# Performance work log

Measured on AMD Instinct MI355X. Metric: run time of the kernel, lower is better.

## Reference

```python
import jax, jax.numpy as jnp
import numpy as np

B, T, NIN, N, NOUT = 64, 512, 64, 1024, 32
DT, TAU = 1.0, 10.0
STATE_STD, RATE_STD, OUT_STD = 0.05, 0.05, 0.05
HIDDEN_G = 1.0


def retanh(x):
    return jnp.maximum(jnp.tanh(x), 0.0)


def setup_inputs() -> dict:
    key = jax.random.key(0)
    ks = jax.random.split(key, 10)
    u = jax.random.normal(ks[0], (B, T, NIN), jnp.float32)
    x_0 = jnp.zeros((N,), jnp.float32)
    state_noise = STATE_STD * jax.random.normal(ks[1], (B, T, N), jnp.float32)
    rate_noise = RATE_STD * jax.random.normal(ks[2], (B, T, N), jnp.float32)
    output_noise = OUT_STD * jax.random.normal(ks[3], (B, T, NOUT), jnp.float32)
    W_in = jax.random.normal(ks[4], (N, NIN), jnp.float32) / np.sqrt(NIN).astype(np.float32)
    b_in = 0.1 + 0.01 * jax.random.normal(ks[5], (N,), jnp.float32)
    W_rec = jax.random.normal(ks[6], (N, N), jnp.float32) * (HIDDEN_G / np.sqrt(N).astype(np.float32))
    W_rec = W_rec * (1.0 - jnp.eye(N, dtype=jnp.float32))  # zero self-connections
    lim = 1.0 / np.sqrt(N).astype(np.float32)
    W_out = jax.random.uniform(ks[7], (NOUT, N), jnp.float32, -lim, lim)
    b_out = jax.random.uniform(ks[8], (NOUT,), jnp.float32, -lim, lim)
    return {"u": u, "x_0": x_0, "state_noise": state_noise, "rate_noise": rate_noise,
            "output_noise": output_noise, "W_in": W_in, "b_in": b_in, "W_rec": W_rec,
            "W_out": W_out, "b_out": b_out}


def reference(u, x_0, state_noise, rate_noise, output_noise, W_in, b_in, W_rec, W_out, b_out):
    alpha = DT / TAU
    # time-major for scan: [T, B, ...]
    u_t = jnp.swapaxes(u, 0, 1)
    sn = jnp.swapaxes(state_noise, 0, 1)
    rn = jnp.swapaxes(rate_noise, 0, 1)
    on = jnp.swapaxes(output_noise, 0, 1)
    x0 = jnp.broadcast_to(x_0, (B, N))
    r0 = retanh(x0)

    def step(carry, inp):
        x, r = carry
        ut, snt, rnt, ont = inp
        x_next = x + alpha * (-x + r @ W_rec.T + ut @ W_in.T + b_in + snt)
        r_next = retanh(x_next) + rnt
        z_next = r_next @ W_out.T + b_out + ont
        return (x_next, r_next), (x_next, r_next, z_next)

    _, (X, R, Z) = jax.lax.scan(step, (x0, r0), (u_t, sn, rn, on))
    # back to batch-major [B, T, ...]
    return (jnp.swapaxes(X, 0, 1), jnp.swapaxes(R, 0, 1), jnp.swapaxes(Z, 0, 1))
```

## Files before the change

kernel.cpp:

```cpp
#include <hip/hip_runtime.h>
#include <hip/hip_bf16.h>
#include <stdint.h>

#define B_    64
#define T_    512
#define NIN_  64
#define N_    1024
#define NOUT_ 32

#define NISL  16
#define BPI   16
#define MB    4
#define COLS  64
#define NT    4
#define KW    256
#define KT    8

#define MAIL_WORDS (NISL * BPI * BPI)

typedef float f32x4 __attribute__((ext_vector_type(4)));
typedef short s16x8 __attribute__((ext_vector_type(8)));

__device__ __forceinline__ unsigned short f2bf(float f) {
  union { float f; unsigned u; } v; v.f = f;
  unsigned r = v.u + 0x7FFFu + ((v.u >> 16) & 1u);
  return (unsigned short)(r >> 16);
}

__device__ __forceinline__ s16x8 cvt8(float4 a, float4 b) {
  s16x8 f;
  f[0] = (short)f2bf(a.x); f[1] = (short)f2bf(a.y);
  f[2] = (short)f2bf(a.z); f[3] = (short)f2bf(a.w);
  f[4] = (short)f2bf(b.x); f[5] = (short)f2bf(b.y);
  f[6] = (short)f2bf(b.z); f[7] = (short)f2bf(b.w);
  return f;
}

#define LD16S(dst, base, OFF) \
  asm volatile("global_load_dwordx4 %0, %1, off offset:" #OFF " sc0 sc1" \
               : "=v"(dst) : "v"(base) : "memory")
#define LDALLS() do { \
  LD16S(afr[0], bp, 0);   LD16S(afr[1], bp, 64);  \
  LD16S(afr[2], bp, 128); LD16S(afr[3], bp, 192); \
  LD16S(afr[4], bp, 256); LD16S(afr[5], bp, 320); \
  LD16S(afr[6], bp, 384); LD16S(afr[7], bp, 448); } while (0)

__global__ __launch_bounds__(256, 1) void rnn_scan(
    const float* __restrict__ U, const float* __restrict__ X0,
    const float* __restrict__ SN, const float* __restrict__ RN,
    const float* __restrict__ Wi, const float* __restrict__ Bi,
    const float* __restrict__ Wr,
    float* __restrict__ X, float* __restrict__ R,
    unsigned* __restrict__ mail, unsigned* __restrict__ ex)
{
  const int bid   = blockIdx.x;
  const int isl   = bid / BPI, slice = bid % BPI;
  const int tid   = threadIdx.x;
  const int wave  = tid >> 6, lane = tid & 63;
  const int l15   = lane & 15, koct = lane >> 4;
  const int colbase = slice * COLS;

  s16x8 bfrag[KT][NT];
#pragma unroll
  for (int kt = 0; kt < KT; ++kt) {
    const int k0 = wave * KW + kt * 32 + koct * 8;
#pragma unroll
    for (int nt = 0; nt < NT; ++nt) {
      const float4* q = (const float4*)(Wr + (size_t)(colbase + nt * 16 + l15) * N_ + k0);
      bfrag[kt][nt] = cvt8(q[0], q[1]);
    }
  }
  s16x8 wifrag[NT];
  if (wave < 2) {
#pragma unroll
    for (int nt = 0; nt < NT; ++nt) {
      const float4* q = (const float4*)(Wi + (size_t)(colbase + nt * 16 + l15) * NIN_ + wave * 32 + koct * 8);
      wifrag[nt] = cvt8(q[0], q[1]);
    }
  }

  const int cc   = lane;
  const int bloc = wave;
  const int bg   = isl * MB + bloc;
  const int nn   = colbase + cc;
  const int abatch = isl * MB + (l15 & 3);

  float x = X0[nn];
  const float bin = Bi[nn];
  const float r0 = fmaxf(tanhf(x), 0.f);

  __shared__ float part[4][COLS][MB];

  const unsigned* const myline = mail + (isl * BPI + slice) * BPI;
  unsigned* const postcol      = mail + isl * BPI * BPI + slice;

  {
    unsigned short h = f2bf(r0);
    unsigned other = __shfl_xor((unsigned)h, 1);
    unsigned vv  = (unsigned)h | (other << 16);
    unsigned vv2 = __shfl_xor(vv, 2);
    if ((lane & 3) == 0) {
      uint64_t q8 = (uint64_t)vv | ((uint64_t)vv2 << 32);
      __hip_atomic_store((uint64_t*)(ex + (size_t)bg * (N_ / 2) + (nn >> 1)), q8,
                         __ATOMIC_RELAXED, __HIP_MEMORY_SCOPE_AGENT);
    }
  }
  __syncthreads();
  if (tid < BPI)
    __hip_atomic_store(postcol + tid * BPI, 1u,
                       __ATOMIC_RELAXED, __HIP_MEMORY_SCOPE_AGENT);

  float pxn = 0.f, prv = 0.f;

  for (int t = 0; t < T_; ++t) {
    const int par = t & 1;
    const size_t row = (size_t)bg * T_ + t;

    const float snv = SN[row * N_ + nn];
    const float rnv = RN[row * N_ + nn];
    float4 uq0, uq1;
    if (wave < 2) {
      const float4* q = (const float4*)(U + ((size_t)(isl * MB + (l15 & 3)) * T_ + t) * NIN_
                                          + wave * 32 + koct * 8);
      uq0 = q[0]; uq1 = q[1];
    }

    {
      const unsigned need = (unsigned)(t + 1);
      for (;;) {
        unsigned fv = __hip_atomic_load(myline + l15, __ATOMIC_RELAXED,
                                        __HIP_MEMORY_SCOPE_AGENT);
        if (__all((int)(fv >= need))) break;
        __builtin_amdgcn_s_sleep(1);
      }
    }

    if (t > 0) {
      X[(row - 1) * N_ + nn] = pxn;
      R[(row - 1) * N_ + nn] = prv;
    }

    const unsigned* bp = ex + (size_t)par * (B_ * (N_ / 2))
                            + (size_t)abatch * (N_ / 2)
                            + ((wave * KW + koct * 8) >> 1);
    s16x8 afr[KT];
    LDALLS();
    asm volatile("s_waitcnt vmcnt(0)" ::: "memory");
    __builtin_amdgcn_sched_barrier(0);

    f32x4 acc[NT];
#pragma unroll
    for (int nt = 0; nt < NT; ++nt) acc[nt] = f32x4{0.f, 0.f, 0.f, 0.f};
#pragma unroll
    for (int kt = 0; kt < KT; ++kt)
#pragma unroll
      for (int nt = 0; nt < NT; ++nt)
        acc[nt] = __builtin_amdgcn_mfma_f32_16x16x32_bf16(afr[kt], bfrag[kt][nt], acc[nt], 0, 0, 0);
    if (wave < 2) {
      s16x8 ua = cvt8(uq0, uq1);
#pragma unroll
      for (int nt = 0; nt < NT; ++nt)
        acc[nt] = __builtin_amdgcn_mfma_f32_16x16x32_bf16(ua, wifrag[nt], acc[nt], 0, 0, 0);
    }

    if (lane < 16) {
#pragma unroll
      for (int nt = 0; nt < NT; ++nt) {
        const int s = (nt * 2 + (lane >> 3)) & 3;
        f32x4 a = acc[nt];
        if (s & 1) a = f32x4{a[1], a[0], a[3], a[2]};
        if (s & 2) a = f32x4{a[2], a[3], a[0], a[1]};
        *(f32x4*)&part[wave][nt * 16 + lane][0] = a;
      }
    }
    __syncthreads();
    const int sr = (cc >> 3) & 3;
    const float mat = part[0][cc][bloc ^ sr] + part[1][cc][bloc ^ sr] +
                      part[2][cc][bloc ^ sr] + part[3][cc][bloc ^ sr];
    const float xn = x + 0.1f * (-x + mat + bin + snv);
    const float rv = fmaxf(tanhf(xn), 0.f) + rnv;
    x = xn;

    {
      unsigned short h = f2bf(rv);
      unsigned other = __shfl_xor((unsigned)h, 1);
      unsigned vv  = (unsigned)h | (other << 16);
      unsigned vv2 = __shfl_xor(vv, 2);
      if ((lane & 3) == 0) {
        uint64_t q8 = (uint64_t)vv | ((uint64_t)vv2 << 32);
        __hip_atomic_store((uint64_t*)(ex + (size_t)(par ^ 1) * (B_ * (N_ / 2)) +
                                       (size_t)bg * (N_ / 2) + (nn >> 1)), q8,
                           __ATOMIC_RELAXED, __HIP_MEMORY_SCOPE_AGENT);
      }
    }
    __syncthreads();
    if (tid < BPI)
      __hip_atomic_store(postcol + tid * BPI, (unsigned)(t + 2),
                         __ATOMIC_RELAXED, __HIP_MEMORY_SCOPE_AGENT);

    pxn = xn; prv = rv;
  }
  {
    const size_t lrow = (size_t)bg * T_ + (T_ - 1);
    X[lrow * N_ + nn] = pxn;
    R[lrow * N_ + nn] = prv;
  }
}

#define TCH 64
__global__ __launch_bounds__(256, 2) void rnn_zout(
    const float* __restrict__ Rm, const float* __restrict__ ON,
    const float* __restrict__ Wo, const float* __restrict__ Bo,
    float* __restrict__ Z)
{
  const int bid = blockIdx.x;
  const int b = bid >> 3, tq = bid & 7;
  const int tid = threadIdx.x;
  const int o = tid & 31, kc = tid >> 5;

  float4 wv[32];
  const float4* wp = (const float4*)(Wo + (size_t)o * N_ + kc * 128);
#pragma unroll
  for (int i = 0; i < 32; ++i) wv[i] = wp[i];
  const float bo = Bo[o];

  __shared__ float Rl[2][N_];
  __shared__ float zred[2][8][32];

  const int t0 = tq * TCH;
  ((float4*)Rl[0])[tid] = ((const float4*)(Rm + ((size_t)b * T_ + t0) * N_))[tid];
  __syncthreads();

  for (int i = 0; i < TCH; ++i) {
    const int cur = i & 1;
    const size_t row = (size_t)b * T_ + t0 + i;
    float4 nx;
    if (i + 1 < TCH)
      nx = ((const float4*)(Rm + (row + 1) * N_))[tid];
    float a0 = 0.f;
#pragma unroll
    for (int j = 0; j < 32; ++j) {
      const float* rp = &Rl[cur][kc * 128 + j * 4];
      a0 += wv[j].x * rp[0] + wv[j].y * rp[1] + wv[j].z * rp[2] + wv[j].w * rp[3];
    }
    if (i + 1 < TCH)
      ((float4*)Rl[cur ^ 1])[tid] = nx;
    zred[cur][kc][o] = a0;
    __syncthreads();
    if (tid < 32) {
      float z = bo;
#pragma unroll
      for (int k = 0; k < 8; ++k) z += zred[cur][k][tid];
      Z[row * NOUT_ + tid] = z + ON[row * NOUT_ + tid];
    }
  }
}

extern "C" void kernel_launch(void* const* d_in, const int* in_sizes, int n_in,
                              void* d_out, int out_size, void* d_ws, size_t ws_size,
                              hipStream_t stream) {
  const float* U  = (const float*)d_in[0];
  const float* X0 = (const float*)d_in[1];
  const float* SN = (const float*)d_in[2];
  const float* RN = (const float*)d_in[3];
  const float* ON = (const float*)d_in[4];
  const float* Wi = (const float*)d_in[5];
  const float* Bi = (const float*)d_in[6];
  const float* Wr = (const float*)d_in[7];
  const float* Wo = (const float*)d_in[8];
  const float* Bo = (const float*)d_in[9];

  float* X = (float*)d_out;
  float* R = X + (size_t)B_ * T_ * N_;
  float* Z = R + (size_t)B_ * T_ * N_;

  unsigned* mail = (unsigned*)d_ws;
  unsigned* ex   = (unsigned*)((char*)d_ws + 65536);

  hipMemsetAsync(mail, 0, MAIL_WORDS * sizeof(unsigned), stream);

  hipLaunchKernelGGL(rnn_scan, dim3(NISL * BPI), dim3(256), 0, stream,
                     U, X0, SN, RN, Wi, Bi, Wr, X, R, mail, ex);
  hipLaunchKernelGGL(rnn_zout, dim3(B_ * (T_ / TCH)), dim3(256), 0, stream,
                     R, ON, Wo, Bo, Z);
}
```

Baseline: 1.519 ms.

## Replace block-level barrier flags with per-wave mailbox flags in RNN scan

Each wave now publishes its own progress flag to every consumer block (64 flags per mailbox line), and consumers poll all 64 lanes. This removes the __syncthreads before signalling so waves can post without waiting for siblings. X/R stores move after the flag post rather than being deferred to the next step. The cost is more flag traffic and wider polling, plus a reliance on s_waitcnt for ordering instead of a block barrier.

```diff
diff --git a/kernel.cpp b/kernel.cpp
--- a/kernel.cpp
+++ b/kernel.cpp
@@ -16,7 +16,7 @@
 #define KW    256
 #define KT    8
 
-#define MAIL_WORDS (NISL * BPI * BPI)
+#define MAIL_WORDS (NISL * BPI * 64)
 
 typedef float f32x4 __attribute__((ext_vector_type(4)));
 typedef short s16x8 __attribute__((ext_vector_type(8)));
@@ -59,6 +59,7 @@
   const int wave  = tid >> 6, lane = tid & 63;
   const int l15   = lane & 15, koct = lane >> 4;
   const int colbase = slice * COLS;
+  const int wid   = slice * 4 + wave;
 
   s16x8 bfrag[KT][NT];
 #pragma unroll
@@ -91,8 +92,7 @@
 
   __shared__ float part[4][COLS][MB];
 
-  const unsigned* const myline = mail + (isl * BPI + slice) * BPI;
-  unsigned* const postcol      = mail + isl * BPI * BPI + slice;
+  const unsigned* const myline = mail + (size_t)(isl * BPI + slice) * 64;
 
   {
     unsigned short h = f2bf(r0);
@@ -105,12 +105,10 @@
                          __ATOMIC_RELAXED, __HIP_MEMORY_SCOPE_AGENT);
     }
   }
-  __syncthreads();
-  if (tid < BPI)
-    __hip_atomic_store(postcol + tid * BPI, 1u,
+  asm volatile("s_waitcnt vmcnt(0)" ::: "memory");
+  if (lane < BPI)
+    __hip_atomic_store(mail + (size_t)(isl * BPI + lane) * 64 + wid, 1u,
                        __ATOMIC_RELAXED, __HIP_MEMORY_SCOPE_AGENT);
-
-  float pxn = 0.f, prv = 0.f;
 
   for (int t = 0; t < T_; ++t) {
     const int par = t & 1;
@@ -128,16 +126,11 @@
     {
       const unsigned need = (unsigned)(t + 1);
       for (;;) {
-        unsigned fv = __hip_atomic_load(myline + l15, __ATOMIC_RELAXED,
+        unsigned fv = __hip_atomic_load(myline + lane, __ATOMIC_RELAXED,
                                         __HIP_MEMORY_SCOPE_AGENT);
         if (__all((int)(fv >= need))) break;
         __builtin_amdgcn_s_sleep(1);
       }
-    }
-
-    if (t > 0) {
-      X[(row - 1) * N_ + nn] = pxn;
-      R[(row - 1) * N_ + nn] = prv;
     }
 
     const unsigned* bp = ex + (size_t)par * (B_ * (N_ / 2))
@@ -193,17 +186,14 @@
                            __ATOMIC_RELAXED, __HIP_MEMORY_SCOPE_AGENT);
       }
     }
-    __syncthreads();
-    if (tid < BPI)
-      __hip_atomic_store(postcol + tid * BPI, (unsigned)(t + 2),
+    asm volatile("s_waitcnt vmcnt(0)" ::: "memory");
+    if (lane < BPI)
+      __hip_atomic_store(mail + (size_t)(isl * BPI + lane) * 64 + wid,
+                         (unsigned)(t + 2),
                          __ATOMIC_RELAXED, __HIP_MEMORY_SCOPE_AGENT);
 
-    pxn = xn; prv = rv;
-  }
-  {
-    const size_t lrow = (size_t)bg * T_ + (T_ - 1);
-    X[lrow * N_ + nn] = pxn;
-    R[lrow * N_ + nn] = prv;
+    X[row * N_ + nn] = xn;
+    R[row * N_ + nn] = rv;
   }
 }
 
```

Measured after the change: 1.992 ms. 1.31x slower.
